# Kernel optimization log

Hardware: AMD Instinct MI355X
Metric: run time of the kernel (lower is better)

## Reference

```python
import jax, jax.numpy as jnp
import numpy as np

EPS = 1e-12  # guard sqrt at zero distance


def setup_inputs() -> dict:
    key = jax.random.key(0)
    k1, k2 = jax.random.split(key)
    B, C, N = 4, 3, 8192
    predict_pc = jax.random.normal(k1, (B, C, N), dtype=jnp.float32)
    gt_pc = jax.random.normal(k2, (B, C, N), dtype=jnp.float32)
    return {"predict_pc": predict_pc, "gt_pc": gt_pc}


def reference(predict_pc, gt_pc):
    # predict_pc: [B, 3, Np], gt_pc: [B, 3, Ng]
    B = gt_pc.shape[0]
    Np = predict_pc.shape[2]
    Ng = gt_pc.shape[2]
    denom = B * (Ng + Np)

    # Pairwise Euclidean distances d[b, n, m] = ||predict[b,:,n] - gt[b,:,m]||
    # via the |p|^2 + |g|^2 - 2 p.g expansion (avoids [B,3,Np,Ng] intermediate).
    p2 = jnp.sum(predict_pc * predict_pc, axis=1)            # [B, Np]
    g2 = jnp.sum(gt_pc * gt_pc, axis=1)                      # [B, Ng]
    dot = jnp.einsum('bcn,bcm->bnm', predict_pc, gt_pc)      # [B, Np, Ng]
    d2 = p2[:, :, None] + g2[:, None, :] - 2.0 * dot         # [B, Np, Ng]
    d = jnp.sqrt(jnp.maximum(d2, EPS))

    # z: for each gt point, distance to nearest predicted point -> min over Np
    z = jnp.min(d, axis=1)   # [B, Ng]
    # z_2: for each predicted point, distance to nearest gt point -> min over Ng
    z2 = jnp.min(d, axis=2)  # [B, Np]

    loss = z.sum() / denom + z2.sum() / denom
    return loss
```

## Files before the change

### kernel.cpp

```cpp
#include <hip/hip_runtime.h>
#include <math.h>


#define B_       4
#define N_       8192
#define THREADS  256
#define RX       8
#define XB       (THREADS * RX)
#define XBLKS    (N_ / XB)
#define NPB      (2 * B_)

typedef float v2f __attribute__((ext_vector_type(2)));

__device__ __forceinline__ v2f pk_fma(v2f a, v2f b, v2f c) {
    v2f d;
    asm("v_pk_fma_f32 %0, %1, %2, %3" : "=v"(d) : "v"(a), "v"(b), "v"(c));
    return d;
}


template<int YSPL>
__global__ __launch_bounds__(THREADS)
void chamfer_sweep_t(const float* __restrict__ P, const float* __restrict__ G,
                     float* __restrict__ partial)
{
    constexpr int YCHUNK = N_ / YSPL;
    __shared__ float4 ytile[2 * (YCHUNK / 2)];

    const int t      = threadIdx.x;
    const int xblk   = blockIdx.x;
    const int ysplit = blockIdx.y;
    const int bz     = blockIdx.z;
    const int pass   = bz >> 2;
    const int b      = bz & 3;

    const float* Xb = (pass ? G : P) + (size_t)b * 3 * N_;
    const float* Yb = (pass ? P : G) + (size_t)b * 3 * N_;

    const int ybase = ysplit * YCHUNK;
    if (t < YCHUNK / 2) {
        const int n0 = ybase + 2 * t;
        float2 x01 = *(const float2*)&Yb[n0];
        float2 y01 = *(const float2*)&Yb[N_ + n0];
        float2 z01 = *(const float2*)&Yb[2 * N_ + n0];
        float w0 = fmaf(x01.x, x01.x, fmaf(y01.x, y01.x, z01.x * z01.x));
        float w1 = fmaf(x01.y, x01.y, fmaf(y01.y, y01.y, z01.y * z01.y));
        ytile[2 * t]     = make_float4(x01.x, x01.y, y01.x, y01.y);
        ytile[2 * t + 1] = make_float4(z01.x, z01.y, w0, w1);
    }

    const int xbase = xblk * XB;
    v2f m2x2[RX], m2y2[RX], m2z2[RX];
    float p2[RX], mn[RX];
#pragma unroll
    for (int r = 0; r < RX; ++r) {
        const int n = xbase + r * THREADS + t;
        float px = Xb[n];
        float py = Xb[N_ + n];
        float pz = Xb[2 * N_ + n];
        p2[r]   = fmaf(px, px, fmaf(py, py, pz * pz));
        float ax = -2.0f * px, ay = -2.0f * py, az = -2.0f * pz;
        m2x2[r] = (v2f){ax, ax};
        m2y2[r] = (v2f){ay, ay};
        m2z2[r] = (v2f){az, az};
        mn[r]   = 3.4e38f;
    }
    __syncthreads();

#pragma unroll 2
    for (int jj = 0; jj < YCHUNK / 2; ++jj) {
        float4 a4 = ytile[2 * jj];
        float4 b4 = ytile[2 * jj + 1];
        v2f gx2 = (v2f){a4.x, a4.y};
        v2f gy2 = (v2f){a4.z, a4.w};
        v2f gz2 = (v2f){b4.x, b4.y};
        v2f gw2 = (v2f){b4.z, b4.w};
#pragma unroll
        for (int r = 0; r < RX; ++r) {
            v2f s = pk_fma(m2z2[r], gz2, gw2);
            s = pk_fma(m2y2[r], gy2, s);
            s = pk_fma(m2x2[r], gx2, s);
            mn[r] = fminf(fminf(mn[r], s.x), s.y);
        }
    }

    float* pout = partial + ((size_t)bz * YSPL + ysplit) * N_ + xbase;
#pragma unroll
    for (int r = 0; r < RX; ++r)
        pout[r * THREADS + t] = fmaxf(mn[r] + p2[r], 1e-12f);
}

template<int YSPL>
__global__ __launch_bounds__(THREADS)
void chamfer_reduce1_t(const float* __restrict__ partial,
                       float* __restrict__ gsum2)
{
    __shared__ float red[THREADS];
    const int g  = blockIdx.x * THREADS + threadIdx.x;
    const int pb = g >> 13;
    const int x  = g & 8191;
    const float* p = partial + (size_t)pb * YSPL * N_ + x;
    float m = p[0];
#pragma unroll
    for (int ys = 1; ys < YSPL; ++ys)
        m = fminf(m, p[(size_t)ys * N_]);
    red[threadIdx.x] = sqrtf(m);
    __syncthreads();
    for (int off = 128; off > 0; off >>= 1) {
        if (threadIdx.x < off) red[threadIdx.x] += red[threadIdx.x + off];
        __syncthreads();
    }
    if (threadIdx.x == 0) gsum2[blockIdx.x] = red[0];
}

__global__ __launch_bounds__(THREADS)
void chamfer_final_kernel(const float* __restrict__ gsum2, float* __restrict__ out)
{
    __shared__ float red[THREADS];
    red[threadIdx.x] = gsum2[threadIdx.x];
    __syncthreads();
    for (int off = 128; off > 0; off >>= 1) {
        if (threadIdx.x < off) red[threadIdx.x] += red[threadIdx.x + off];
        __syncthreads();
    }
    if (threadIdx.x == 0) out[0] = red[0] * (1.0f / 65536.0f);
}

#define LRX      8
#define LXB      (THREADS * LRX)
#define LXBLKS   (N_ / LXB)
#define LYSPL    32
#define LYCHUNK  (N_ / LYSPL)
#define LNGROUPS (2 * B_ * LXBLKS)
#define POISON   0xAAAAAAAAu

__global__ __launch_bounds__(THREADS)
void chamfer_fused_kernel(const float* __restrict__ P, const float* __restrict__ G,
                          unsigned* __restrict__ mins, unsigned* __restrict__ gcnt,
                          unsigned* __restrict__ fcnt, float* __restrict__ gsum,
                          float* __restrict__ out)
{
    __shared__ float4 ytile[2 * (LYCHUNK / 2)];
    __shared__ float red[THREADS];
    __shared__ unsigned s_ticket;

    const int t      = threadIdx.x;
    const int xblk   = blockIdx.x;
    const int ysplit = blockIdx.y;
    const int bz     = blockIdx.z;
    const int pass   = bz >> 2;
    const int b      = bz & 3;
    const int gid    = bz * LXBLKS + xblk;

    const float* Xb = (pass ? G : P) + (size_t)b * 3 * N_;
    const float* Yb = (pass ? P : G) + (size_t)b * 3 * N_;

    const int ybase = ysplit * LYCHUNK;
    if (t < LYCHUNK / 2) {
        const int n0 = ybase + 2 * t;
        float2 x01 = *(const float2*)&Yb[n0];
        float2 y01 = *(const float2*)&Yb[N_ + n0];
        float2 z01 = *(const float2*)&Yb[2 * N_ + n0];
        float w0 = fmaf(x01.x, x01.x, fmaf(y01.x, y01.x, z01.x * z01.x));
        float w1 = fmaf(x01.y, x01.y, fmaf(y01.y, y01.y, z01.y * z01.y));
        ytile[2 * t]     = make_float4(x01.x, x01.y, y01.x, y01.y);
        ytile[2 * t + 1] = make_float4(z01.x, z01.y, w0, w1);
    }

    const int xbase = xblk * LXB;
    v2f m2x2[LRX], m2y2[LRX], m2z2[LRX];
    float p2[LRX], mn[LRX];
#pragma unroll
    for (int r = 0; r < LRX; ++r) {
        const int n = xbase + r * THREADS + t;
        float px = Xb[n];
        float py = Xb[N_ + n];
        float pz = Xb[2 * N_ + n];
        p2[r]   = fmaf(px, px, fmaf(py, py, pz * pz));
        float ax = -2.0f * px, ay = -2.0f * py, az = -2.0f * pz;
        m2x2[r] = (v2f){ax, ax};
        m2y2[r] = (v2f){ay, ay};
        m2z2[r] = (v2f){az, az};
        mn[r]   = 3.4e38f;
    }
    __syncthreads();

#pragma unroll 2
    for (int jj = 0; jj < LYCHUNK / 2; ++jj) {
        float4 a4 = ytile[2 * jj];
        float4 b4 = ytile[2 * jj + 1];
        v2f gx2 = (v2f){a4.x, a4.y};
        v2f gy2 = (v2f){a4.z, a4.w};
        v2f gz2 = (v2f){b4.x, b4.y};
        v2f gw2 = (v2f){b4.z, b4.w};
#pragma unroll
        for (int r = 0; r < LRX; ++r) {
            v2f s = pk_fma(m2z2[r], gz2, gw2);
            s = pk_fma(m2y2[r], gy2, s);
            s = pk_fma(m2x2[r], gx2, s);
            mn[r] = fminf(fminf(mn[r], s.x), s.y);
        }
    }

    unsigned* mybase = mins + (size_t)(pass * B_ + b) * N_ + xbase;
#pragma unroll
    for (int r = 0; r < LRX; ++r) {
        float v = fmaxf(mn[r] + p2[r], 1e-12f);
        atomicMin(&mybase[r * THREADS + t], __float_as_uint(v));
    }

    __syncthreads();
    if (t == 0) {
        __threadfence();
        s_ticket = atomicAdd(&gcnt[gid], 1u);
    }
    __syncthreads();
    if (s_ticket != POISON + (unsigned)(LYSPL - 1)) return;

    __threadfence();
    const uint4* vmin = (const uint4*)(mins + (size_t)(pass * B_ + b) * N_ + xbase);
    uint4 q0 = vmin[t];
    uint4 q1 = vmin[THREADS + t];
    float a = sqrtf(__uint_as_float(q0.x)) + sqrtf(__uint_as_float(q0.y))
            + sqrtf(__uint_as_float(q0.z)) + sqrtf(__uint_as_float(q0.w))
            + sqrtf(__uint_as_float(q1.x)) + sqrtf(__uint_as_float(q1.y))
            + sqrtf(__uint_as_float(q1.z)) + sqrtf(__uint_as_float(q1.w));
    red[t] = a;
    __syncthreads();
    for (int off = 128; off > 0; off >>= 1) {
        if (t < off) red[t] += red[t + off];
        __syncthreads();
    }
    if (t == 0) {
        gsum[gid] = red[0];
        __threadfence();
        s_ticket = atomicAdd(fcnt, 1u);
    }
    __syncthreads();
    if (s_ticket != POISON + (unsigned)(LNGROUPS - 1)) return;

    __threadfence();
    red[t] = (t < LNGROUPS) ? gsum[t] : 0.0f;
    __syncthreads();
    for (int off = 128; off > 0; off >>= 1) {
        if (t < off) red[t] += red[t + off];
        __syncthreads();
    }
    if (t == 0) out[0] = red[0] * (1.0f / 65536.0f);
}

extern "C" void kernel_launch(void* const* d_in, const int* in_sizes, int n_in,
                              void* d_out, int out_size, void* d_ws, size_t ws_size,
                              hipStream_t stream)
{
    const float* P = (const float*)d_in[0];
    const float* G = (const float*)d_in[1];
    float* out = (float*)d_out;

    const size_t need64 = ((size_t)NPB * 64 * N_ + 256) * 4;
    const size_t need32 = ((size_t)NPB * 32 * N_ + 256) * 4;

    if (ws_size >= need64) {
        float* partial = (float*)d_ws;
        float* gsum2   = partial + (size_t)NPB * 64 * N_;
        chamfer_sweep_t<64><<<dim3(XBLKS, 64, NPB), THREADS, 0, stream>>>(P, G, partial);
        chamfer_reduce1_t<64><<<dim3(256), THREADS, 0, stream>>>(partial, gsum2);
        chamfer_final_kernel<<<dim3(1), THREADS, 0, stream>>>(gsum2, out);
    } else if (ws_size >= need32) {
        float* partial = (float*)d_ws;
        float* gsum2   = partial + (size_t)NPB * 32 * N_;
        chamfer_sweep_t<32><<<dim3(XBLKS, 32, NPB), THREADS, 0, stream>>>(P, G, partial);
        chamfer_reduce1_t<32><<<dim3(256), THREADS, 0, stream>>>(partial, gsum2);
        chamfer_final_kernel<<<dim3(1), THREADS, 0, stream>>>(gsum2, out);
    } else {
        unsigned* w    = (unsigned*)d_ws;
        unsigned* mins = w;
        unsigned* gcnt = w + 65536;
        unsigned* fcnt = w + 65600;
        float*    gsum = (float*)(w + 65664);
        dim3 grid(LXBLKS, LYSPL, NPB);
        chamfer_fused_kernel<<<grid, THREADS, 0, stream>>>(P, G, mins, gcnt, fcnt, gsum, out);
    }
}
```

Measured before the change: 104.0 us.

## Use min3, software-prefetch the shared tile, and vectorize the reduction kernel

Result: no change. 103.8 us (-0.1%).

```diff
diff --git a/kernel.cpp b/kernel.cpp
--- a/kernel.cpp
+++ b/kernel.cpp
@@ -9,6 +9,7 @@
 #define XB       (THREADS * RX)
 #define XBLKS    (N_ / XB)
 #define NPB      (2 * B_)
+#define RTHREADS 128
 
 typedef float v2f __attribute__((ext_vector_type(2)));
 
@@ -18,6 +19,12 @@
     return d;
 }
 
+__device__ __forceinline__ float min3f(float a, float b, float c) {
+    float d;
+    asm("v_min3_f32 %0, %1, %2, %3" : "=v"(d) : "v"(a), "v"(b), "v"(c));
+    return d;
+}
+
 
 template<int YSPL>
 __global__ __launch_bounds__(THREADS)
@@ -25,7 +32,8 @@
                      float* __restrict__ partial)
 {
     constexpr int YCHUNK = N_ / YSPL;
-    __shared__ float4 ytile[2 * (YCHUNK / 2)];
+    constexpr int NJJ    = YCHUNK / 2;
+    __shared__ v2f ytile[4 * NJJ + 8];
 
     const int t      = threadIdx.x;
     const int xblk   = blockIdx.x;
@@ -38,27 +46,30 @@
     const float* Yb = (pass ? P : G) + (size_t)b * 3 * N_;
 
     const int ybase = ysplit * YCHUNK;
-    if (t < YCHUNK / 2) {
+    if (t < NJJ) {
         const int n0 = ybase + 2 * t;
         float2 x01 = *(const float2*)&Yb[n0];
         float2 y01 = *(const float2*)&Yb[N_ + n0];
         float2 z01 = *(const float2*)&Yb[2 * N_ + n0];
         float w0 = fmaf(x01.x, x01.x, fmaf(y01.x, y01.x, z01.x * z01.x));
         float w1 = fmaf(x01.y, x01.y, fmaf(y01.y, y01.y, z01.y * z01.y));
-        ytile[2 * t]     = make_float4(x01.x, x01.y, y01.x, y01.y);
-        ytile[2 * t + 1] = make_float4(z01.x, z01.y, w0, w1);
+        ytile[4 * t + 0] = (v2f){x01.x, x01.y};
+        ytile[4 * t + 1] = (v2f){y01.x, y01.y};
+        ytile[4 * t + 2] = (v2f){z01.x, z01.y};
+        ytile[4 * t + 3] = (v2f){w0, w1};
+    } else if (t < NJJ + 8) {
+        ytile[4 * NJJ + (t - NJJ)] = (v2f){0.0f, 0.0f};
     }
 
     const int xbase = xblk * XB;
     v2f m2x2[RX], m2y2[RX], m2z2[RX];
-    float p2[RX], mn[RX];
+    float mn[RX];
 #pragma unroll
     for (int r = 0; r < RX; ++r) {
         const int n = xbase + r * THREADS + t;
         float px = Xb[n];
         float py = Xb[N_ + n];
         float pz = Xb[2 * N_ + n];
-        p2[r]   = fmaf(px, px, fmaf(py, py, pz * pz));
         float ax = -2.0f * px, ay = -2.0f * py, az = -2.0f * pz;
         m2x2[r] = (v2f){ax, ax};
         m2y2[r] = (v2f){ay, ay};
@@ -67,59 +78,68 @@
     }
     __syncthreads();
 
+    v2f cx0 = ytile[0], cy0 = ytile[1], cz0 = ytile[2], cw0 = ytile[3];
+    v2f cx1 = ytile[4], cy1 = ytile[5], cz1 = ytile[6], cw1 = ytile[7];
 #pragma unroll 2
-    for (int jj = 0; jj < YCHUNK / 2; ++jj) {
-        float4 a4 = ytile[2 * jj];
-        float4 b4 = ytile[2 * jj + 1];
-        v2f gx2 = (v2f){a4.x, a4.y};
-        v2f gy2 = (v2f){a4.z, a4.w};
-        v2f gz2 = (v2f){b4.x, b4.y};
-        v2f gw2 = (v2f){b4.z, b4.w};
+    for (int jj = 0; jj < NJJ; ++jj) {
+        const int pf = 4 * jj + 8;
+        v2f nx = ytile[pf + 0];
+        v2f ny = ytile[pf + 1];
+        v2f nz = ytile[pf + 2];
+        v2f nw = ytile[pf + 3];
 #pragma unroll
         for (int r = 0; r < RX; ++r) {
-            v2f s = pk_fma(m2z2[r], gz2, gw2);
-            s = pk_fma(m2y2[r], gy2, s);
-            s = pk_fma(m2x2[r], gx2, s);
-            mn[r] = fminf(fminf(mn[r], s.x), s.y);
+            v2f s = pk_fma(m2z2[r], cz0, cw0);
+            s = pk_fma(m2y2[r], cy0, s);
+            s = pk_fma(m2x2[r], cx0, s);
+            mn[r] = min3f(mn[r], s.x, s.y);
         }
+        cx0 = cx1; cy0 = cy1; cz0 = cz1; cw0 = cw1;
+        cx1 = nx;  cy1 = ny;  cz1 = nz;  cw1 = nw;
     }
 
     float* pout = partial + ((size_t)bz * YSPL + ysplit) * N_ + xbase;
 #pragma unroll
-    for (int r = 0; r < RX; ++r)
-        pout[r * THREADS + t] = fmaxf(mn[r] + p2[r], 1e-12f);
+    for (int r = 0; r < RX; ++r) {
+        float ax = m2x2[r].x, ay = m2y2[r].x, az = m2z2[r].x;
+        float p2 = 0.25f * fmaf(ax, ax, fmaf(ay, ay, az * az));
+        pout[r * THREADS + t] = fmaxf(mn[r] + p2, 1e-12f);
+    }
 }
 
 template<int YSPL>
-__global__ __launch_bounds__(THREADS)
+__global__ __launch_bounds__(RTHREADS)
 void chamfer_reduce1_t(const float* __restrict__ partial,
                        float* __restrict__ gsum2)
 {
-    __shared__ float red[THREADS];
-    const int g  = blockIdx.x * THREADS + threadIdx.x;
-    const int pb = g >> 13;
-    const int x  = g & 8191;
-    const float* p = partial + (size_t)pb * YSPL * N_ + x;
-    float m = p[0];
-#pragma unroll
-    for (int ys = 1; ys < YSPL; ++ys)
-        m = fminf(m, p[(size_t)ys * N_]);
-    red[threadIdx.x] = sqrtf(m);
-    __syncthreads();
-    for (int off = 128; off > 0; off >>= 1) {
+    __shared__ float red[RTHREADS];
+    const int g  = blockIdx.x * RTHREADS + threadIdx.x;
+    const int pb = g >> 11;
+    const int xq = g & 2047;
+    const float4* p = (const float4*)(partial + (size_t)pb * YSPL * N_) + xq;
+    float4 m = p[0];
+#pragma unroll
+    for (int ys = 1; ys < YSPL; ++ys) {
+        float4 v = p[(size_t)ys * (N_ / 4)];
+        m.x = fminf(m.x, v.x); m.y = fminf(m.y, v.y);
+        m.z = fminf(m.z, v.z); m.w = fminf(m.w, v.w);
+    }
+    red[threadIdx.x] = sqrtf(m.x) + sqrtf(m.y) + sqrtf(m.z) + sqrtf(m.w);
+    __syncthreads();
+    for (int off = RTHREADS / 2; off > 0; off >>= 1) {
         if (threadIdx.x < off) red[threadIdx.x] += red[threadIdx.x + off];
         __syncthreads();
     }
     if (threadIdx.x == 0) gsum2[blockIdx.x] = red[0];
 }
 
-__global__ __launch_bounds__(THREADS)
+__global__ __launch_bounds__(RTHREADS)
 void chamfer_final_kernel(const float* __restrict__ gsum2, float* __restrict__ out)
 {
-    __shared__ float red[THREADS];
+    __shared__ float red[RTHREADS];
     red[threadIdx.x] = gsum2[threadIdx.x];
     __syncthreads();
-    for (int off = 128; off > 0; off >>= 1) {
+    for (int off = RTHREADS / 2; off > 0; off >>= 1) {
         if (threadIdx.x < off) red[threadIdx.x] += red[threadIdx.x + off];
         __syncthreads();
     }
@@ -264,14 +284,14 @@
         float* partial = (float*)d_ws;
         float* gsum2   = partial + (size_t)NPB * 64 * N_;
         chamfer_sweep_t<64><<<dim3(XBLKS, 64, NPB), THREADS, 0, stream>>>(P, G, partial);
-        chamfer_reduce1_t<64><<<dim3(256), THREADS, 0, stream>>>(partial, gsum2);
-        chamfer_final_kernel<<<dim3(1), THREADS, 0, stream>>>(gsum2, out);
+        chamfer_reduce1_t<64><<<dim3(128), RTHREADS, 0, stream>>>(partial, gsum2);
+        chamfer_final_kernel<<<dim3(1), RTHREADS, 0, stream>>>(gsum2, out);
     } else if (ws_size >= need32) {
         float* partial = (float*)d_ws;
         float* gsum2   = partial + (size_t)NPB * 32 * N_;
         chamfer_sweep_t<32><<<dim3(XBLKS, 32, NPB), THREADS, 0, stream>>>(P, G, partial);
-        chamfer_reduce1_t<32><<<dim3(256), THREADS, 0, stream>>>(partial, gsum2);
-        chamfer_final_kernel<<<dim3(1), THREADS, 0, stream>>>(gsum2, out);
+        chamfer_reduce1_t<32><<<dim3(128), RTHREADS, 0, stream>>>(partial, gsum2);
+        chamfer_final_kernel<<<dim3(1), RTHREADS, 0, stream>>>(gsum2, out);
     } else {
         unsigned* w    = (unsigned*)d_ws;
         unsigned* mins = w;
```
